# Performance work log

Measured on AMD Instinct MI355X. Metric: run time of the kernel, lower is better.

Reference implementation:

```python
import jax, jax.numpy as jnp
import numpy as np
from jax import lax

# Mamba2 hyperparameters (mamba_ssm defaults scaled to d_model=512)
D_MODEL = 512
EXPAND = 2
D_INNER = EXPAND * D_MODEL          # 1024
HEADDIM = 64
NHEADS = D_INNER // HEADDIM         # 16
D_STATE = 64
NGROUPS = 1
D_CONV = 4
CONV_DIM = D_INNER + 2 * NGROUPS * D_STATE   # 1152
D_IN_PROJ = 2 * D_INNER + 2 * NGROUPS * D_STATE + NHEADS  # 2192
EPS = 1e-5


def setup_inputs() -> dict:
    key = jax.random.key(0)
    ks = jax.random.split(key, 8)
    x = jax.random.normal(ks[0], (4, 2044, D_MODEL), jnp.float32)
    in_proj_w = jax.random.normal(ks[1], (D_MODEL, D_IN_PROJ), jnp.float32) * 0.02
    conv_w = jax.random.normal(ks[2], (CONV_DIM, 1, D_CONV), jnp.float32) * 0.2  # depthwise [O,I/g,K]
    conv_b = jnp.zeros((CONV_DIM,), jnp.float32)
    dt_bias = jax.random.uniform(ks[3], (NHEADS,), jnp.float32, 0.0, 0.1)
    A_log = jnp.log(jax.random.uniform(ks[4], (NHEADS,), jnp.float32, 1.0, 16.0))
    D_skip = jnp.ones((NHEADS,), jnp.float32)
    norm_w = jnp.ones((D_INNER,), jnp.float32)
    out_proj_w = jax.random.normal(ks[5], (D_INNER, D_MODEL), jnp.float32) * 0.02
    return {
        "x": x, "in_proj_w": in_proj_w, "conv_w": conv_w, "conv_b": conv_b,
        "dt_bias": dt_bias, "A_log": A_log, "D_skip": D_skip,
        "norm_w": norm_w, "out_proj_w": out_proj_w,
    }


def _mamba2(x, in_proj_w, conv_w, conv_b, dt_bias, A_log, D_skip, norm_w, out_proj_w):
    B, Lp, _ = x.shape
    zxbcdt = x @ in_proj_w                                  # [B,Lp,D_IN_PROJ]
    z = zxbcdt[..., :D_INNER]                               # gate
    xBC = zxbcdt[..., D_INNER:D_INNER + CONV_DIM]
    dt = zxbcdt[..., D_INNER + CONV_DIM:]                   # [B,Lp,H]

    # causal depthwise conv over time, then silu
    xBC_c = lax.conv_general_dilated(
        xBC.transpose(0, 2, 1), conv_w, window_strides=(1,),
        padding=[(D_CONV - 1, 0)], feature_group_count=CONV_DIM,
        dimension_numbers=("NCH", "OIH", "NCH"))
    xBC = jax.nn.silu(xBC_c.transpose(0, 2, 1) + conv_b)    # [B,Lp,CONV_DIM]

    xs = xBC[..., :D_INNER]
    Bm = xBC[..., D_INNER:D_INNER + NGROUPS * D_STATE]      # [B,Lp,N] (g=1)
    Cm = xBC[..., D_INNER + NGROUPS * D_STATE:]             # [B,Lp,N]

    dt = jax.nn.softplus(dt + dt_bias)                      # [B,Lp,H]
    A = -jnp.exp(A_log)                                     # [H]
    xh = xs.reshape(B, Lp, NHEADS, HEADDIM)                 # [B,Lp,H,P]

    decay = jnp.exp(dt * A)                                 # [B,Lp,H]
    dtx = dt[..., None] * xh                                # [B,Lp,H,P]

    def step(h, inp):
        dec_t, dtx_t, B_t, C_t = inp                        # [B,H],[B,H,P],[B,N],[B,N]
        h = dec_t[:, :, None, None] * h + dtx_t[..., None] * B_t[:, None, None, :]
        y_t = jnp.einsum("bhpn,bn->bhp", h, C_t)
        return h, y_t

    h0 = jnp.zeros((B, NHEADS, HEADDIM, D_STATE), x.dtype)
    _, ys = lax.scan(step, h0, (decay.transpose(1, 0, 2),
                                dtx.transpose(1, 0, 2, 3),
                                Bm.transpose(1, 0, 2),
                                Cm.transpose(1, 0, 2)))
    y = ys.transpose(1, 0, 2, 3) + D_skip[None, None, :, None] * xh  # [B,Lp,H,P]
    y = y.reshape(B, Lp, D_INNER)

    # gated RMSNorm (RMSNormGated): gate first, then normalize
    y = y * jax.nn.silu(z)
    y = y * lax.rsqrt(jnp.mean(y * y, axis=-1, keepdims=True) + EPS) * norm_w
    return y @ out_proj_w                                   # [B,Lp,D_MODEL]


def reference(x, in_proj_w, conv_w, conv_b, dt_bias, A_log, D_skip, norm_w, out_proj_w):
    # MemoryEfficientMamba wrapper: pad seq_len to multiple of 8, run mamba, slice back
    L = x.shape[1]
    pad = (-L) % 8
    xp = jnp.pad(x, ((0, 0), (0, pad), (0, 0))) if pad else x
    out = _mamba2(xp, in_proj_w, conv_w, conv_b, dt_bias, A_log, D_skip, norm_w, out_proj_w)
    return out[:, :L, :]
```

## Files before the change

kernel.cpp:

```cpp
#include <hip/hip_runtime.h>
#include <hip/hip_bf16.h>
#include <math.h>
#include <string.h>

#define BATCH   4
#define SEQ     2044
#define DMODEL  512
#define DINNER  1024
#define NHEADS  16
#define HEADDIM 64
#define DSTATE  64
#define CONVDIM 1152
#define DINPROJ 2192
#define ZW      2176
#define NROWS   (BATCH*SEQ)
#define Q       64
#define NCHUNK  32

typedef __attribute__((ext_vector_type(8))) short bf16x8;
typedef __attribute__((ext_vector_type(4))) short short4v;
typedef __attribute__((ext_vector_type(4))) float f32x4;

#define MFMA(a,b,c) __builtin_amdgcn_mfma_f32_16x16x32_bf16((a),(b),(c),0,0,0)

__device__ inline short f2bf(float f) {
    __hip_bfloat16 h = __float2bfloat16(f);
    short s; memcpy(&s, &h, 2); return s;
}
__device__ inline float bf2f(short s) {
    unsigned u = ((unsigned)(unsigned short)s) << 16;
    float f; memcpy(&f, &u, 4); return f;
}
__device__ inline float bf2f_lo(unsigned u) {
    unsigned v = u << 16; float f; memcpy(&f, &v, 4); return f;
}
__device__ inline float bf2f_hi(unsigned u) {
    unsigned v = u & 0xffff0000u; float f; memcpy(&f, &v, 4); return f;
}

__device__ __forceinline__ void gload16(const short* g, short* l) {
    __builtin_amdgcn_global_load_lds(
        (const __attribute__((address_space(1))) void*)g,
        (__attribute__((address_space(3))) void*)l, 16, 0, 0);
}

__global__ __launch_bounds__(256) void convert_bf16_kernel(const float* __restrict__ in,
                                                           short* __restrict__ out, int n8) {
    int i = blockIdx.x * 256 + threadIdx.x;
    if (i >= n8) return;
    float4 v0 = *((const float4*)in + i * 2);
    float4 v1 = *((const float4*)in + i * 2 + 1);
    short t[8];
    t[0]=f2bf(v0.x); t[1]=f2bf(v0.y); t[2]=f2bf(v0.z); t[3]=f2bf(v0.w);
    t[4]=f2bf(v1.x); t[5]=f2bf(v1.y); t[6]=f2bf(v1.z); t[7]=f2bf(v1.w);
    *((bf16x8*)out + i) = *(const bf16x8*)t;
}

__global__ __launch_bounds__(256) void transpose_cvt_kernel(const float* __restrict__ in,
                                                            short* __restrict__ out,
                                                            int R, int Cc, int ldi) {
    __shared__ float tile[64][65];
    const int bx = blockIdx.x * 64;
    const int by = blockIdx.y * 64;
    const int tid = threadIdx.x;
#pragma unroll
    for (int i = 0; i < 16; i++) {
        int idx = tid + i * 256; int r = idx >> 6, c = idx & 63;
        float v = 0.f;
        if (by + r < R && bx + c < Cc) v = in[(size_t)(by + r) * ldi + bx + c];
        tile[r][c] = v;
    }
    __syncthreads();
#pragma unroll
    for (int i = 0; i < 16; i++) {
        int idx = tid + i * 256; int c = idx >> 6, r = idx & 63;
        if (bx + c < Cc && by + r < R)
            out[(size_t)(bx + c) * R + by + r] = f2bf(tile[r][c]);
    }
}

template<bool BF16OUT>
__global__ __launch_bounds__(256) void gemm_bf16(const short* __restrict__ A,
                                                 const short* __restrict__ Bt,
                                                 void* __restrict__ Cv,
                                                 int M, int N, int K,
                                                 int Nbf, float* __restrict__ dtout,
                                                 const float* __restrict__ dt_bias,
                                                 const float* __restrict__ A_log) {
    __shared__ short As[64][64];
    __shared__ short Bs[64][64];
    const int tid = threadIdx.x;
    const int wave = tid >> 6, lane = tid & 63;
    const int bm = blockIdx.x * 64, bn = blockIdx.y * 64;
    const int lane15 = lane & 15;
    const int kgrp = lane >> 4;
    const int srow = lane >> 3;
    const int scol = (lane & 7) ^ srow;
    const int r7 = lane15 & 7;

    f32x4 acc[4];
#pragma unroll
    for (int j = 0; j < 4; j++) acc[j] = (f32x4){0.f, 0.f, 0.f, 0.f};

    const short* Ab = A + (size_t)(bm + wave * 16 + srow) * K + scol * 8;
    const short* Bb = Bt + (size_t)(bn + wave * 16 + srow) * K + scol * 8;

    for (int kk = 0; kk < K; kk += 64) {
        gload16(Ab + kk,                 &As[wave * 16][0]);
        gload16(Ab + 8 * (size_t)K + kk, &As[wave * 16 + 8][0]);
        gload16(Bb + kk,                 &Bs[wave * 16][0]);
        gload16(Bb + 8 * (size_t)K + kk, &Bs[wave * 16 + 8][0]);
        __syncthreads();
        const int arow = (wave << 4) + lane15;
        bf16x8 a0 = *(const bf16x8*)&As[arow][(kgrp ^ r7) * 8];
        bf16x8 a1 = *(const bf16x8*)&As[arow][((kgrp + 4) ^ r7) * 8];
#pragma unroll
        for (int j = 0; j < 4; j++) {
            const int brow = (j << 4) + lane15;
            bf16x8 b0 = *(const bf16x8*)&Bs[brow][(kgrp ^ r7) * 8];
            bf16x8 b1 = *(const bf16x8*)&Bs[brow][((kgrp + 4) ^ r7) * 8];
            acc[j] = MFMA(a0, b0, acc[j]);
            acc[j] = MFMA(a1, b1, acc[j]);
        }
        __syncthreads();
    }
    const int crow = bm + (wave << 4) + ((lane >> 4) << 2);
    const int ccol0 = bn + lane15;
    const bool has_dt = BF16OUT && (dtout != nullptr) && (bn + 64 > Nbf);
    if (!has_dt) {
#pragma unroll
        for (int j = 0; j < 4; j++) {
            int gn = ccol0 + j * 16;
            if (gn >= N) continue;
#pragma unroll
            for (int i = 0; i < 4; i++) {
                int gm = crow + i;
                if (gm >= M) continue;
                float v = acc[j][i];
                if (BF16OUT) ((short*)Cv)[(size_t)gm * Nbf + gn] = f2bf(v);
                else         ((float*)Cv)[(size_t)gm * N + gn] = v;
            }
        }
    } else {
        const int ndt = N - Nbf;
#pragma unroll
        for (int j = 0; j < 4; j++) {
            int gn = ccol0 + j * 16;
            if (gn >= N) continue;
#pragma unroll
            for (int i = 0; i < 4; i++) {
                int gm = crow + i;
                if (gm >= M) continue;
                float v = acc[j][i];
                if (gn >= Nbf) {
                    int h = gn - Nbf;
                    float v2 = v + dt_bias[h];
                    float sp = (v2 > 20.f) ? v2 : log1pf(expf(v2));
                    dtout[(size_t)gm * ndt + h] = sp * (-expf(A_log[h]));
                } else {
                    ((short*)Cv)[(size_t)gm * Nbf + gn] = f2bf(v);
                }
            }
        }
    }
}

__global__ __launch_bounds__(256) void conv_silu_kernel(const short* __restrict__ zxb,
                                                        const float* __restrict__ conv_w,
                                                        const float* __restrict__ conv_b,
                                                        short* __restrict__ convo) {
    const int CH2 = CONVDIM / 2;
    int idx = blockIdx.x * 256 + threadIdx.x;
    if (idx >= BATCH * (SEQ/4) * CH2) return;
    int cpair = idx % CH2;
    int q = idx / CH2;
    int b = q / (SEQ/4);
    int t0 = (q % (SEQ/4)) * 4;
    int c = cpair * 2;
    const size_t base = ((size_t)b * SEQ + t0) * ZW + DINNER + c;
    float4 wv0 = *(const float4*)&conv_w[c * 4];
    float4 wv1 = *(const float4*)&conv_w[c * 4 + 4];
    float x0[7], x1[7];
#pragma unroll
    for (int i = 0; i < 7; i++) {
        int t = t0 - 3 + i;
        if (t >= 0) {
            unsigned u = *(const unsigned*)&zxb[base + (size_t)(i - 3) * ZW];
            x0[i] = bf2f_lo(u); x1[i] = bf2f_hi(u);
        } else { x0[i] = 0.f; x1[i] = 0.f; }
    }
    const float b0 = conv_b[c], b1 = conv_b[c + 1];
    const size_t obase = ((size_t)b * SEQ + t0) * CONVDIM + c;
#pragma unroll
    for (int i = 0; i < 4; i++) {
        float a0 = b0 + x0[i]*wv0.x + x0[i+1]*wv0.y + x0[i+2]*wv0.z + x0[i+3]*wv0.w;
        float a1 = b1 + x1[i]*wv1.x + x1[i+1]*wv1.y + x1[i+2]*wv1.z + x1[i+3]*wv1.w;
        float s0 = a0 / (1.f + expf(-a0));
        float s1 = a1 / (1.f + expf(-a1));
        unsigned o = (unsigned)(unsigned short)f2bf(s0) |
                     ((unsigned)(unsigned short)f2bf(s1) << 16);
        *(unsigned*)&convo[obase + (size_t)i * CONVDIM] = o;
    }
}

__global__ __launch_bounds__(256) void chunk_state_kernel(
    const short* __restrict__ convo,
    const float* __restrict__ lab,
    const float* __restrict__ A_log,
    short* __restrict__ Sbf,
    float* __restrict__ atot)
{
    const int blk = blockIdx.x;
    const int h  = blk & 15;
    const int bc = blk >> 4;
    const int c  = bc & (NCHUNK - 1);
    const int b  = bc >> 5;
    const int t0 = c * Q;
    const int len = min(Q, SEQ - t0);
    const int tid = threadIdx.x;
    const int wave = tid >> 6, lane = tid & 63;
    const size_t rowbase = (size_t)b * SEQ + t0;

    __shared__ short Xt[64][72];
    __shared__ short Bw[64][72];
    __shared__ float sw[64];

    if (tid < 64) {
        const float nAinv = -expf(-A_log[h]);
        float lav = 0.f;
        if (tid < len) lav = lab[(rowbase + tid) * NHEADS + h];
        float dtv = lav * nAinv;
        float v = lav;
#pragma unroll
        for (int off = 1; off < 64; off <<= 1) {
            float nb = __shfl_up(v, off);
            if (lane >= off) v += nb;
        }
        float last = __shfl(v, 63);
        sw[tid] = expf(last - v) * dtv;
        if (tid == 63) atot[blk] = expf(last);
    }
    __syncthreads();

    {
        const int r = tid >> 2, qq = tid & 3;
        const bf16x8 zz = {0,0,0,0,0,0,0,0};
        bf16x8 b0 = zz, b1 = zz, x0 = zz, x1 = zz;
        if (r < len) {
            const short* row = convo + (rowbase + r) * CONVDIM;
            b0 = *(const bf16x8*)&row[1024 + qq*16];
            b1 = *(const bf16x8*)&row[1024 + qq*16 + 8];
            x0 = *(const bf16x8*)&row[h*64 + qq*16];
            x1 = *(const bf16x8*)&row[h*64 + qq*16 + 8];
        }
        const float wsc = sw[r];
        short bs[16], xs[16];
        *(bf16x8*)&bs[0] = b0; *(bf16x8*)&bs[8] = b1;
        *(bf16x8*)&xs[0] = x0; *(bf16x8*)&xs[8] = x1;
#pragma unroll
        for (int i = 0; i < 16; i++) Xt[qq*16+i][r] = xs[i];
#pragma unroll
        for (int i = 0; i < 16; i++) Bw[qq*16+i][r] = f2bf(bf2f(bs[i]) * wsc);
    }
    __syncthreads();

    const int arow = (wave << 4) + (lane & 15);
    const int koff = (lane >> 4) << 3;
    const int trow0 = (wave << 4) + ((lane >> 4) << 2);
    const int scol = lane & 15;

    f32x4 sacc[4];
#pragma unroll
    for (int j = 0; j < 4; j++) sacc[j] = (f32x4){0.f,0.f,0.f,0.f};
    {
        bf16x8 a0 = *(const bf16x8*)&Xt[arow][koff];
        bf16x8 a1 = *(const bf16x8*)&Xt[arow][32 + koff];
#pragma unroll
        for (int j = 0; j < 4; j++) {
            const int brow = (j << 4) + (lane & 15);
            bf16x8 b0 = *(const bf16x8*)&Bw[brow][koff];
            bf16x8 b1 = *(const bf16x8*)&Bw[brow][32 + koff];
            sacc[j] = MFMA(a0, b0, sacc[j]);
            sacc[j] = MFMA(a1, b1, sacc[j]);
        }
    }
    const size_t sbase = (size_t)blk * 4096;
#pragma unroll
    for (int j = 0; j < 4; j++) {
        int n = j * 16 + scol;
#pragma unroll
        for (int i = 0; i < 4; i++) {
            int p = trow0 + i;
            Sbf[sbase + p * 64 + n] = f2bf(sacc[j][i]);
        }
    }
}

__global__ __launch_bounds__(256) void chunk_state_scan_kernel(
    const short* __restrict__ Sbf, const float* __restrict__ atot,
    short* __restrict__ Hbf)
{
    int e = blockIdx.x * 256 + threadIdx.x;
    int bh = e >> 11;
    int el = (e & 2047) * 2;
    int b = bh >> 4, h = bh & 15;
    float H0 = 0.f, H1 = 0.f;
    for (int c = 0; c < NCHUNK; c++) {
        int blk = (b * NCHUNK + c) * NHEADS + h;
        size_t off = (size_t)blk * 4096 + el;
        unsigned sv = *(const unsigned*)&Sbf[off];
        unsigned hv = (unsigned)(unsigned short)f2bf(H0) |
                      ((unsigned)(unsigned short)f2bf(H1) << 16);
        *(unsigned*)&Hbf[off] = hv;
        float at = atot[blk];
        H0 = at * H0 + bf2f_lo(sv);
        H1 = at * H1 + bf2f_hi(sv);
    }
}

__global__ __launch_bounds__(256) void chunk_yfuse_kernel(
    const short* __restrict__ convo,
    const float* __restrict__ lab,
    const float* __restrict__ A_log,
    const float* __restrict__ D_skip,
    const short* __restrict__ Hbf,
    short* __restrict__ ybf)
{
    const int blk = blockIdx.x;
    const int h  = blk & 15;
    const int bc = blk >> 4;
    const int c  = bc & (NCHUNK - 1);
    const int b  = bc >> 5;
    const int t0 = c * Q;
    const int len = min(Q, SEQ - t0);
    const int tid = threadIdx.x;
    const int wave = tid >> 6, lane = tid & 63;
    const size_t rowbase = (size_t)b * SEQ + t0;

    __shared__ short Ct[64][72];
    __shared__ short Bt2[64][72];
    __shared__ short Xt[64][72];
    __shared__ short Hs[64][72];
    __shared__ float cum[64], sdt[64];

    if (tid < 64) {
        const float nAinv = -expf(-A_log[h]);
        float lav = 0.f;
        if (tid < len) lav = lab[(rowbase + tid) * NHEADS + h];
        float dtv = lav * nAinv;
        float v = lav;
#pragma unroll
        for (int off = 1; off < 64; off <<= 1) {
            float nb = __shfl_up(v, off);
            if (lane >= off) v += nb;
        }
        cum[tid] = v; sdt[tid] = dtv;
    }
    __syncthreads();

    {
        const int r = tid >> 2, qq = tid & 3;
        const bf16x8 zz = {0,0,0,0,0,0,0,0};
        bf16x8 c0 = zz, c1 = zz, b0 = zz, b1 = zz, x0 = zz, x1 = zz;
        if (r < len) {
            const short* row = convo + (rowbase + r) * CONVDIM;
            c0 = *(const bf16x8*)&row[1088 + qq*16];
            c1 = *(const bf16x8*)&row[1088 + qq*16 + 8];
            b0 = *(const bf16x8*)&row[1024 + qq*16];
            b1 = *(const bf16x8*)&row[1024 + qq*16 + 8];
            x0 = *(const bf16x8*)&row[h*64 + qq*16];
            x1 = *(const bf16x8*)&row[h*64 + qq*16 + 8];
        }
        *(bf16x8*)&Ct[r][qq*16]    = c0; *(bf16x8*)&Ct[r][qq*16+8]  = c1;
        *(bf16x8*)&Bt2[r][qq*16]   = b0; *(bf16x8*)&Bt2[r][qq*16+8] = b1;
        short xs[16];
        *(bf16x8*)&xs[0] = x0; *(bf16x8*)&xs[8] = x1;
#pragma unroll
        for (int i = 0; i < 16; i++) Xt[qq*16+i][r] = xs[i];
        const size_t hbase = (size_t)blk * 4096;
        bf16x8 h0 = *(const bf16x8*)&Hbf[hbase + r*64 + qq*16];
        bf16x8 h1 = *(const bf16x8*)&Hbf[hbase + r*64 + qq*16 + 8];
        *(bf16x8*)&Hs[r][qq*16]   = h0;
        *(bf16x8*)&Hs[r][qq*16+8] = h1;
    }
    __syncthreads();

    const int arow = (wave << 4) + (lane & 15);
    const int koff = (lane >> 4) << 3;
    const int trow0 = (wave << 4) + ((lane >> 4) << 2);
    const int scol = lane & 15;

    f32x4 eacc[4], iacc[4];
#pragma unroll
    for (int j = 0; j < 4; j++) { eacc[j] = (f32x4){0.f,0.f,0.f,0.f}; iacc[j] = (f32x4){0.f,0.f,0.f,0.f}; }
    {
        bf16x8 a0 = *(const bf16x8*)&Ct[arow][koff];
        bf16x8 a1 = *(const bf16x8*)&Ct[arow][32 + koff];
#pragma unroll
        for (int j = 0; j < 4; j++) {
            const int brow = (j << 4) + (lane & 15);
            bf16x8 b0 = *(const bf16x8*)&Bt2[brow][koff];
            bf16x8 b1 = *(const bf16x8*)&Bt2[brow][32 + koff];
            eacc[j] = MFMA(a0, b0, eacc[j]);
            eacc[j] = MFMA(a1, b1, eacc[j]);
            bf16x8 h0 = *(const bf16x8*)&Hs[brow][koff];
            bf16x8 h1 = *(const bf16x8*)&Hs[brow][32 + koff];
            iacc[j] = MFMA(a0, h0, iacc[j]);
            iacc[j] = MFMA(a1, h1, iacc[j]);
        }
    }
    short ebf[4][4];
#pragma unroll
    for (int j = 0; j < 4; j++) {
        int s = j * 16 + scol;
#pragma unroll
        for (int i = 0; i < 4; i++) {
            int t = trow0 + i;
            float val = 0.f;
            if (s <= t) val = eacc[j][i] * expf(cum[t] - cum[s]) * sdt[s];
            ebf[j][i] = f2bf(val);
        }
    }
    __syncthreads();
#pragma unroll
    for (int j = 0; j < 4; j++)
#pragma unroll
        for (int i = 0; i < 4; i++)
            Ct[trow0 + i][j * 16 + scol] = ebf[j][i];
    __syncthreads();

    f32x4 yacc[4];
#pragma unroll
    for (int j = 0; j < 4; j++) yacc[j] = (f32x4){0.f,0.f,0.f,0.f};
    {
        bf16x8 a0 = *(const bf16x8*)&Ct[arow][koff];
        bf16x8 a1 = *(const bf16x8*)&Ct[arow][32 + koff];
#pragma unroll
        for (int j = 0; j < 4; j++) {
            const int brow = (j << 4) + (lane & 15);
            bf16x8 b0 = *(const bf16x8*)&Xt[brow][koff];
            bf16x8 b1 = *(const bf16x8*)&Xt[brow][32 + koff];
            yacc[j] = MFMA(a0, b0, yacc[j]);
            yacc[j] = MFMA(a1, b1, yacc[j]);
        }
    }
    const float dsk = D_skip[h];
#pragma unroll
    for (int j = 0; j < 4; j++) {
        int p = j * 16 + scol;
#pragma unroll
        for (int i = 0; i < 4; i++) {
            int t = trow0 + i;
            if (t < len) {
                float ce = expf(cum[t]);
                float xv = bf2f(Xt[p][t]);
                float val = yacc[j][i] + ce * iacc[j][i] + dsk * xv;
                ybf[(rowbase + t) * DINNER + h * 64 + p] = f2bf(val);
            }
        }
    }
}

__global__ __launch_bounds__(256) void gate_rmsnorm_kernel(short* __restrict__ y,
                                                           const short* __restrict__ zxb,
                                                           const float* __restrict__ norm_w) {
    const int m = blockIdx.x;
    const int tid = threadIdx.x;
    const int c = tid * 4;
    short4v yv = *(const short4v*)&y[(size_t)m * DINNER + c];
    short4v zv = *(const short4v*)&zxb[(size_t)m * ZW + c];
    float vals[4];
    float ss = 0.f;
#pragma unroll
    for (int i = 0; i < 4; i++) {
        float v = bf2f(yv[i]);
        float z = bf2f(zv[i]);
        float g = v * (z / (1.f + expf(-z)));
        vals[i] = g;
        ss += g * g;
    }
#pragma unroll
    for (int mask = 1; mask < 64; mask <<= 1) ss += __shfl_xor(ss, mask);
    __shared__ float red[4];
    if ((tid & 63) == 0) red[tid >> 6] = ss;
    __syncthreads();
    float tot = red[0] + red[1] + red[2] + red[3];
    float scale = rsqrtf(tot / 1024.f + 1e-5f);
    short4v ov;
#pragma unroll
    for (int i = 0; i < 4; i++) ov[i] = f2bf(vals[i] * scale * norm_w[c + i]);
    *(short4v*)&y[(size_t)m * DINNER + c] = ov;
}

extern "C" void kernel_launch(void* const* d_in, const int* in_sizes, int n_in,
                              void* d_out, int out_size, void* d_ws, size_t ws_size,
                              hipStream_t stream) {
    const float* x          = (const float*)d_in[0];
    const float* in_proj_w  = (const float*)d_in[1];
    const float* conv_w     = (const float*)d_in[2];
    const float* conv_b     = (const float*)d_in[3];
    const float* dt_bias    = (const float*)d_in[4];
    const float* A_log      = (const float*)d_in[5];
    const float* D_skip     = (const float*)d_in[6];
    const float* norm_w     = (const float*)d_in[7];
    const float* out_proj_w = (const float*)d_in[8];
    float* out = (float*)d_out;

    short* zxb   = (short*)d_ws;
    short* convo = zxb + (size_t)NROWS * ZW;
    short* ybf   = convo + (size_t)NROWS * CONVDIM;
    short* Hbf   = ybf + (size_t)NROWS * DINNER;
    short* Sbf   = Hbf + (size_t)2048 * 4096;
    float* lab   = (float*)(Sbf + (size_t)2048 * 4096);
    float* atotb = lab + (size_t)NROWS * NHEADS;
    short* w2t   = (short*)(atotb + 2048);
    short* xb  = convo;
    short* w1t = xb + (size_t)NROWS * DMODEL;

    convert_bf16_kernel<<<(NROWS * DMODEL / 8 + 255) / 256, 256, 0, stream>>>(x, xb, NROWS * DMODEL / 8);
    {
        dim3 g((DINPROJ + 63) / 64, (DMODEL + 63) / 64);
        transpose_cvt_kernel<<<g, 256, 0, stream>>>(in_proj_w, w1t, DMODEL, DINPROJ, DINPROJ);
    }
    {
        dim3 g((DMODEL + 63) / 64, (DINNER + 63) / 64);
        transpose_cvt_kernel<<<g, 256, 0, stream>>>(out_proj_w, w2t, DINNER, DMODEL, DMODEL);
    }

    {
        dim3 g((NROWS + 63) / 64, (DINPROJ + 63) / 64);
        gemm_bf16<true><<<g, 256, 0, stream>>>(xb, w1t, zxb, NROWS, DINPROJ, DMODEL,
                                               ZW, lab, dt_bias, A_log);
    }

    {
        int tot = BATCH * (SEQ / 4) * (CONVDIM / 2);
        conv_silu_kernel<<<(tot + 255) / 256, 256, 0, stream>>>(zxb, conv_w, conv_b, convo);
    }

    chunk_state_kernel<<<BATCH * NCHUNK * NHEADS, 256, 0, stream>>>(
        convo, lab, A_log, Sbf, atotb);

    chunk_state_scan_kernel<<<(64 * 2048) / 256, 256, 0, stream>>>(Sbf, atotb, Hbf);

    chunk_yfuse_kernel<<<BATCH * NCHUNK * NHEADS, 256, 0, stream>>>(
        convo, lab, A_log, D_skip, Hbf, ybf);

    gate_rmsnorm_kernel<<<NROWS, 256, 0, stream>>>(ybf, zxb, norm_w);

    {
        dim3 g((NROWS + 63) / 64, (DMODEL + 63) / 64);
        gemm_bf16<false><<<g, 256, 0, stream>>>(ybf, w2t, out, NROWS, DMODEL, DINNER,
                                                DMODEL, nullptr, nullptr, nullptr);
    }
}
```

Before: 139.9 us.

## Fuse causal conv+SiLU into chunk state and y kernels, drop conv kernel

Removes the standalone conv_silu kernel and its intermediate convo buffer. The chunk_state and chunk_yfuse kernels now compute the depthwise causal conv plus SiLU directly from the in-projection output, reading 4 time-shifted rows, with conv weights staged in shared memory. The intent is to save one launch and a full write and re-read of the conv output. In exchange the conv is recomputed in both kernels, each row is read 4 times, and the B/C conv work is redone for every head. Separately, the H state fragments in yfuse are loaded straight into registers instead of staged through LDS.

Result: slower. 171.8 us (+22.8%).

```diff
diff --git a/kernel.cpp b/kernel.cpp
--- a/kernel.cpp
+++ b/kernel.cpp
@@ -30,12 +30,6 @@
 __device__ inline float bf2f(short s) {
     unsigned u = ((unsigned)(unsigned short)s) << 16;
     float f; memcpy(&f, &u, 4); return f;
-}
-__device__ inline float bf2f_lo(unsigned u) {
-    unsigned v = u << 16; float f; memcpy(&f, &v, 4); return f;
-}
-__device__ inline float bf2f_hi(unsigned u) {
-    unsigned v = u & 0xffff0000u; float f; memcpy(&f, &v, 4); return f;
 }
 
 __device__ __forceinline__ void gload16(const short* g, short* l) {
@@ -165,48 +159,12 @@
     }
 }
 
-__global__ __launch_bounds__(256) void conv_silu_kernel(const short* __restrict__ zxb,
-                                                        const float* __restrict__ conv_w,
-                                                        const float* __restrict__ conv_b,
-                                                        short* __restrict__ convo) {
-    const int CH2 = CONVDIM / 2;
-    int idx = blockIdx.x * 256 + threadIdx.x;
-    if (idx >= BATCH * (SEQ/4) * CH2) return;
-    int cpair = idx % CH2;
-    int q = idx / CH2;
-    int b = q / (SEQ/4);
-    int t0 = (q % (SEQ/4)) * 4;
-    int c = cpair * 2;
-    const size_t base = ((size_t)b * SEQ + t0) * ZW + DINNER + c;
-    float4 wv0 = *(const float4*)&conv_w[c * 4];
-    float4 wv1 = *(const float4*)&conv_w[c * 4 + 4];
-    float x0[7], x1[7];
-#pragma unroll
-    for (int i = 0; i < 7; i++) {
-        int t = t0 - 3 + i;
-        if (t >= 0) {
-            unsigned u = *(const unsigned*)&zxb[base + (size_t)(i - 3) * ZW];
-            x0[i] = bf2f_lo(u); x1[i] = bf2f_hi(u);
-        } else { x0[i] = 0.f; x1[i] = 0.f; }
-    }
-    const float b0 = conv_b[c], b1 = conv_b[c + 1];
-    const size_t obase = ((size_t)b * SEQ + t0) * CONVDIM + c;
-#pragma unroll
-    for (int i = 0; i < 4; i++) {
-        float a0 = b0 + x0[i]*wv0.x + x0[i+1]*wv0.y + x0[i+2]*wv0.z + x0[i+3]*wv0.w;
-        float a1 = b1 + x1[i]*wv1.x + x1[i+1]*wv1.y + x1[i+2]*wv1.z + x1[i+3]*wv1.w;
-        float s0 = a0 / (1.f + expf(-a0));
-        float s1 = a1 / (1.f + expf(-a1));
-        unsigned o = (unsigned)(unsigned short)f2bf(s0) |
-                     ((unsigned)(unsigned short)f2bf(s1) << 16);
-        *(unsigned*)&convo[obase + (size_t)i * CONVDIM] = o;
-    }
-}
-
 __global__ __launch_bounds__(256) void chunk_state_kernel(
-    const short* __restrict__ convo,
+    const short* __restrict__ zxb,
     const float* __restrict__ lab,
     const float* __restrict__ A_log,
+    const float* __restrict__ conv_w,
+    const float* __restrict__ conv_b,
     short* __restrict__ Sbf,
     float* __restrict__ atot)
 {
@@ -224,7 +182,15 @@
     __shared__ short Xt[64][72];
     __shared__ short Bw[64][72];
     __shared__ float sw[64];
-
+    __shared__ float cwS[128][4];
+    __shared__ float cbS[128];
+
+    if (tid < 128) {
+        int ch = (tid < 64) ? (h * 64 + tid) : (1024 + (tid - 64));
+        float4 w4 = *(const float4*)&conv_w[ch * 4];
+        cwS[tid][0] = w4.x; cwS[tid][1] = w4.y; cwS[tid][2] = w4.z; cwS[tid][3] = w4.w;
+        cbS[tid] = conv_b[ch];
+    }
     if (tid < 64) {
         const float nAinv = -expf(-A_log[h]);
         float lav = 0.f;
@@ -244,23 +210,42 @@
 
     {
         const int r = tid >> 2, qq = tid & 3;
-        const bf16x8 zz = {0,0,0,0,0,0,0,0};
-        bf16x8 b0 = zz, b1 = zz, x0 = zz, x1 = zz;
+        float xacc[16], bacc[16];
+#pragma unroll
+        for (int i = 0; i < 16; i++) {
+            xacc[i] = cbS[qq * 16 + i];
+            bacc[i] = cbS[64 + qq * 16 + i];
+        }
         if (r < len) {
-            const short* row = convo + (rowbase + r) * CONVDIM;
-            b0 = *(const bf16x8*)&row[1024 + qq*16];
-            b1 = *(const bf16x8*)&row[1024 + qq*16 + 8];
-            x0 = *(const bf16x8*)&row[h*64 + qq*16];
-            x1 = *(const bf16x8*)&row[h*64 + qq*16 + 8];
+#pragma unroll
+            for (int k = 0; k < 4; k++) {
+                int t = t0 + r - 3 + k;
+                if (t >= 0) {
+                    const short* rp = zxb + ((size_t)b * SEQ + t) * ZW;
+                    short xs_[16], bs_[16];
+                    *(bf16x8*)&xs_[0] = *(const bf16x8*)&rp[DINNER + h*64 + qq*16];
+                    *(bf16x8*)&xs_[8] = *(const bf16x8*)&rp[DINNER + h*64 + qq*16 + 8];
+                    *(bf16x8*)&bs_[0] = *(const bf16x8*)&rp[DINNER + 1024 + qq*16];
+                    *(bf16x8*)&bs_[8] = *(const bf16x8*)&rp[DINNER + 1024 + qq*16 + 8];
+#pragma unroll
+                    for (int i = 0; i < 16; i++) {
+                        xacc[i] += bf2f(xs_[i]) * cwS[qq*16 + i][k];
+                        bacc[i] += bf2f(bs_[i]) * cwS[64 + qq*16 + i][k];
+                    }
+                }
+            }
         }
         const float wsc = sw[r];
-        short bs[16], xs[16];
-        *(bf16x8*)&bs[0] = b0; *(bf16x8*)&bs[8] = b1;
-        *(bf16x8*)&xs[0] = x0; *(bf16x8*)&xs[8] = x1;
-#pragma unroll
-        for (int i = 0; i < 16; i++) Xt[qq*16+i][r] = xs[i];
-#pragma unroll
-        for (int i = 0; i < 16; i++) Bw[qq*16+i][r] = f2bf(bf2f(bs[i]) * wsc);
+#pragma unroll
+        for (int i = 0; i < 16; i++) {
+            float xr = 0.f, br = 0.f;
+            if (r < len) {
+                xr = xacc[i] / (1.f + expf(-xacc[i]));
+                br = bacc[i] / (1.f + expf(-bacc[i]));
+            }
+            Xt[qq*16 + i][r] = f2bf(xr);
+            Bw[qq*16 + i][r] = f2bf(br * wsc);
+        }
     }
     __syncthreads();
 
@@ -313,15 +298,17 @@
                       ((unsigned)(unsigned short)f2bf(H1) << 16);
         *(unsigned*)&Hbf[off] = hv;
         float at = atot[blk];
-        H0 = at * H0 + bf2f_lo(sv);
-        H1 = at * H1 + bf2f_hi(sv);
+        H0 = at * H0 + ((float)({ unsigned v = sv << 16; float ff; memcpy(&ff, &v, 4); ff; }));
+        H1 = at * H1 + ((float)({ unsigned v = sv & 0xffff0000u; float ff; memcpy(&ff, &v, 4); ff; }));
     }
 }
 
 __global__ __launch_bounds__(256) void chunk_yfuse_kernel(
-    const short* __restrict__ convo,
+    const short* __restrict__ zxb,
     const float* __restrict__ lab,
     const float* __restrict__ A_log,
+    const float* __restrict__ conv_w,
+    const float* __restrict__ conv_b,
     const float* __restrict__ D_skip,
     const short* __restrict__ Hbf,
     short* __restrict__ ybf)
@@ -340,9 +327,19 @@
     __shared__ short Ct[64][72];
     __shared__ short Bt2[64][72];
     __shared__ short Xt[64][72];
-    __shared__ short Hs[64][72];
     __shared__ float cum[64], sdt[64];
-
+    __shared__ float cwS[192][4];
+    __shared__ float cbS[192];
+
+    const int lane15 = lane & 15;
+    const int koff = (lane >> 4) << 3;
+
+    if (tid < 192) {
+        int ch = (tid < 64) ? (h * 64 + tid) : (960 + tid);
+        float4 w4 = *(const float4*)&conv_w[ch * 4];
+        cwS[tid][0] = w4.x; cwS[tid][1] = w4.y; cwS[tid][2] = w4.z; cwS[tid][3] = w4.w;
+        cbS[tid] = conv_b[ch];
+    }
     if (tid < 64) {
         const float nAinv = -expf(-A_log[h]);
         float lav = 0.f;
@@ -356,39 +353,73 @@
         }
         cum[tid] = v; sdt[tid] = dtv;
     }
+
+    bf16x8 hf0[4], hf1[4];
+    {
+        const size_t hbase = (size_t)blk * 4096;
+#pragma unroll
+        for (int j = 0; j < 4; j++) {
+            int brow = (j << 4) + lane15;
+            hf0[j] = *(const bf16x8*)&Hbf[hbase + brow * 64 + koff];
+            hf1[j] = *(const bf16x8*)&Hbf[hbase + brow * 64 + koff + 32];
+        }
+    }
     __syncthreads();
 
     {
         const int r = tid >> 2, qq = tid & 3;
-        const bf16x8 zz = {0,0,0,0,0,0,0,0};
-        bf16x8 c0 = zz, c1 = zz, b0 = zz, b1 = zz, x0 = zz, x1 = zz;
+        float xacc[16], bacc[16], cacc[16];
+#pragma unroll
+        for (int i = 0; i < 16; i++) {
+            xacc[i] = cbS[qq * 16 + i];
+            bacc[i] = cbS[64 + qq * 16 + i];
+            cacc[i] = cbS[128 + qq * 16 + i];
+        }
         if (r < len) {
-            const short* row = convo + (rowbase + r) * CONVDIM;
-            c0 = *(const bf16x8*)&row[1088 + qq*16];
-            c1 = *(const bf16x8*)&row[1088 + qq*16 + 8];
-            b0 = *(const bf16x8*)&row[1024 + qq*16];
-            b1 = *(const bf16x8*)&row[1024 + qq*16 + 8];
-            x0 = *(const bf16x8*)&row[h*64 + qq*16];
-            x1 = *(const bf16x8*)&row[h*64 + qq*16 + 8];
-        }
-        *(bf16x8*)&Ct[r][qq*16]    = c0; *(bf16x8*)&Ct[r][qq*16+8]  = c1;
-        *(bf16x8*)&Bt2[r][qq*16]   = b0; *(bf16x8*)&Bt2[r][qq*16+8] = b1;
-        short xs[16];
-        *(bf16x8*)&xs[0] = x0; *(bf16x8*)&xs[8] = x1;
-#pragma unroll
-        for (int i = 0; i < 16; i++) Xt[qq*16+i][r] = xs[i];
-        const size_t hbase = (size_t)blk * 4096;
-        bf16x8 h0 = *(const bf16x8*)&Hbf[hbase + r*64 + qq*16];
-        bf16x8 h1 = *(const bf16x8*)&Hbf[hbase + r*64 + qq*16 + 8];
-        *(bf16x8*)&Hs[r][qq*16]   = h0;
-        *(bf16x8*)&Hs[r][qq*16+8] = h1;
-    }
-    __syncthreads();
-
-    const int arow = (wave << 4) + (lane & 15);
-    const int koff = (lane >> 4) << 3;
+#pragma unroll
+            for (int k = 0; k < 4; k++) {
+                int t = t0 + r - 3 + k;
+                if (t >= 0) {
+                    const short* rp = zxb + ((size_t)b * SEQ + t) * ZW;
+                    short xs_[16], bs_[16], cs_[16];
+                    *(bf16x8*)&xs_[0] = *(const bf16x8*)&rp[DINNER + h*64 + qq*16];
+                    *(bf16x8*)&xs_[8] = *(const bf16x8*)&rp[DINNER + h*64 + qq*16 + 8];
+                    *(bf16x8*)&bs_[0] = *(const bf16x8*)&rp[2048 + qq*16];
+                    *(bf16x8*)&bs_[8] = *(const bf16x8*)&rp[2048 + qq*16 + 8];
+                    *(bf16x8*)&cs_[0] = *(const bf16x8*)&rp[2112 + qq*16];
+                    *(bf16x8*)&cs_[8] = *(const bf16x8*)&rp[2112 + qq*16 + 8];
+#pragma unroll
+                    for (int i = 0; i < 16; i++) {
+                        xacc[i] += bf2f(xs_[i]) * cwS[qq*16 + i][k];
+                        bacc[i] += bf2f(bs_[i]) * cwS[64 + qq*16 + i][k];
+                        cacc[i] += bf2f(cs_[i]) * cwS[128 + qq*16 + i][k];
+                    }
+                }
+            }
+        }
+        short cv_[16], bv_[16];
+#pragma unroll
+        for (int i = 0; i < 16; i++) {
+            float xr = 0.f, br = 0.f, cr = 0.f;
+            if (r < len) {
+                xr = xacc[i] / (1.f + expf(-xacc[i]));
+                br = bacc[i] / (1.f + expf(-bacc[i]));
+                cr = cacc[i] / (1.f + expf(-cacc[i]));
+            }
+            Xt[qq*16 + i][r] = f2bf(xr);
+            bv_[i] = f2bf(br);
+            cv_[i] = f2bf(cr);
+        }
+        *(bf16x8*)&Ct[r][qq*16]     = *(const bf16x8*)&cv_[0];
+        *(bf16x8*)&Ct[r][qq*16+8]   = *(const bf16x8*)&cv_[8];
+        *(bf16x8*)&Bt2[r][qq*16]    = *(const bf16x8*)&bv_[0];
+        *(bf16x8*)&Bt2[r][qq*16+8]  = *(const bf16x8*)&bv_[8];
+    }
+    __syncthreads();
+
+    const int arow = (wave << 4) + lane15;
     const int trow0 = (wave << 4) + ((lane >> 4) << 2);
-    const int scol = lane & 15;
+    const int scol = lane15;
 
     f32x4 eacc[4], iacc[4];
 #pragma unroll
@@ -398,15 +429,13 @@
         bf16x8 a1 = *(const bf16x8*)&Ct[arow][32 + koff];
 #pragma unroll
         for (int j = 0; j < 4; j++) {
-            const int brow = (j << 4) + (lane & 15);
+            const int brow = (j << 4) + lane15;
             bf16x8 b0 = *(const bf16x8*)&Bt2[brow][koff];
             bf16x8 b1 = *(const bf16x8*)&Bt2[brow][32 + koff];
             eacc[j] = MFMA(a0, b0, eacc[j]);
             eacc[j] = MFMA(a1, b1, eacc[j]);
-            bf16x8 h0 = *(const bf16x8*)&Hs[brow][koff];
-            bf16x8 h1 = *(const bf16x8*)&Hs[brow][32 + koff];
-            iacc[j] = MFMA(a0, h0, iacc[j]);
-            iacc[j] = MFMA(a1, h1, iacc[j]);
+            iacc[j] = MFMA(a0, hf0[j], iacc[j]);
+            iacc[j] = MFMA(a1, hf1[j], iacc[j]);
         }
     }
     short ebf[4][4];
@@ -437,7 +466,7 @@
         bf16x8 a1 = *(const bf16x8*)&Ct[arow][32 + koff];
 #pragma unroll
         for (int j = 0; j < 4; j++) {
-            const int brow = (j << 4) + (lane & 15);
+            const int brow = (j << 4) + lane15;
             bf16x8 b0 = *(const bf16x8*)&Xt[brow][koff];
             bf16x8 b1 = *(const bf16x8*)&Xt[brow][32 + koff];
             yacc[j] = MFMA(a0, b0, yacc[j]);
@@ -507,14 +536,14 @@
     float* out = (float*)d_out;
 
     short* zxb   = (short*)d_ws;
-    short* convo = zxb + (size_t)NROWS * ZW;
-    short* ybf   = convo + (size_t)NROWS * CONVDIM;
+    short* scratch = zxb + (size_t)NROWS * ZW;
+    short* ybf   = scratch + (size_t)NROWS * CONVDIM;
     short* Hbf   = ybf + (size_t)NROWS * DINNER;
     short* Sbf   = Hbf + (size_t)2048 * 4096;
     float* lab   = (float*)(Sbf + (size_t)2048 * 4096);
     float* atotb = lab + (size_t)NROWS * NHEADS;
     short* w2t   = (short*)(atotb + 2048);
-    short* xb  = convo;
+    short* xb  = scratch;
     short* w1t = xb + (size_t)NROWS * DMODEL;
 
     convert_bf16_kernel<<<(NROWS * DMODEL / 8 + 255) / 256, 256, 0, stream>>>(x, xb, NROWS * DMODEL / 8);
@@ -533,18 +562,13 @@
                                                ZW, lab, dt_bias, A_log);
     }
 
-    {
-        int tot = BATCH * (SEQ / 4) * (CONVDIM / 2);
-        conv_silu_kernel<<<(tot + 255) / 256, 256, 0, stream>>>(zxb, conv_w, conv_b, convo);
-    }
-
     chunk_state_kernel<<<BATCH * NCHUNK * NHEADS, 256, 0, stream>>>(
-        convo, lab, A_log, Sbf, atotb);
+        zxb, lab, A_log, conv_w, conv_b, Sbf, atotb);
 
     chunk_state_scan_kernel<<<(64 * 2048) / 256, 256, 0, stream>>>(Sbf, atotb, Hbf);
 
     chunk_yfuse_kernel<<<BATCH * NCHUNK * NHEADS, 256, 0, stream>>>(
-        convo, lab, A_log, D_skip, Hbf, ybf);
+        zxb, lab, A_log, conv_w, conv_b, D_skip, Hbf, ybf);
 
     gate_rmsnorm_kernel<<<NROWS, 256, 0, stream>>>(ybf, zxb, norm_w);
 
```
